# Performance work log

Hardware: AMD Instinct MI355X
Metric: run time of the kernel (lower is better)

The kernel has to match this reference:

```python
import jax, jax.numpy as jnp
import numpy as np

N = 30000          # num nodes
E = 480000         # num edges (before self-loops)
D_MODEL = 128
HEADS = 8
HEAD_DIM = D_MODEL // HEADS  # 16
LAYERS = 7
NUM_LABELS = 2
NEG_SLOPE = 0.2


def setup_inputs() -> dict:
    key = jax.random.key(0)
    ks = jax.random.split(key, 10)
    s = 0.05
    x = jax.random.normal(ks[0], (N, D_MODEL), dtype=jnp.float32)
    edge_index = jax.random.randint(ks[1], (2, E), 0, N, dtype=jnp.int64)
    Wl = jax.random.normal(ks[2], (LAYERS, D_MODEL, D_MODEL), dtype=jnp.float32) * s
    bl = jnp.zeros((LAYERS, D_MODEL), dtype=jnp.float32)
    Wr = jax.random.normal(ks[3], (LAYERS, D_MODEL, D_MODEL), dtype=jnp.float32) * s
    br = jnp.zeros((LAYERS, D_MODEL), dtype=jnp.float32)
    att = jax.random.normal(ks[4], (LAYERS, HEADS, HEAD_DIM), dtype=jnp.float32) * s
    bias = jnp.zeros((LAYERS, D_MODEL), dtype=jnp.float32)
    W_out = jax.random.normal(ks[5], (D_MODEL, 1), dtype=jnp.float32) * s
    b_out = jnp.zeros((1,), dtype=jnp.float32)
    return {"x": x, "edge_index": edge_index, "Wl": Wl, "bl": bl,
            "Wr": Wr, "br": br, "att": att, "bias": bias,
            "W_out": W_out, "b_out": b_out}


def _gatv2_layer(x, Wl, bl, Wr, br, att, bias, src, dst):
    # x: [N, d]; src/dst: [E'] (with self-loops). GATv2 (dropout off / eval).
    xl = (x @ Wl + bl).reshape(N, HEADS, HEAD_DIM)  # source transform
    xr = (x @ Wr + br).reshape(N, HEADS, HEAD_DIM)  # target transform
    m = xl[src] + xr[dst]                           # [E', H, D]
    e = jnp.einsum('ehd,hd->eh', jax.nn.leaky_relu(m, NEG_SLOPE), att)  # [E', H]
    # segment softmax over destination nodes (self-loops => no empty segments)
    emax = jax.ops.segment_max(e, dst, num_segments=N)  # [N, H]
    ee = jnp.exp(e - emax[dst])
    denom = jax.ops.segment_sum(ee, dst, num_segments=N)  # [N, H]
    alpha = ee / (denom[dst] + 1e-16)                      # [E', H]
    out = jax.ops.segment_sum(alpha[:, :, None] * xl[src], dst, num_segments=N)
    return out.reshape(N, D_MODEL) + bias


def reference(x, edge_index, Wl, bl, Wr, br, att, bias, W_out, b_out):
    loops = jnp.arange(N, dtype=edge_index.dtype)
    src = jnp.concatenate([edge_index[0], loops])  # add_self_loops=True (PyG default)
    dst = jnp.concatenate([edge_index[1], loops])
    for i in range(LAYERS):
        x = _gatv2_layer(x, Wl[i], bl[i], Wr[i], br[i], att[i], bias[i], src, dst)
    y = x @ W_out + b_out            # [N, 1]
    return y[:NUM_LABELS, 0].reshape(1, -1)  # [1, num_labels]
```

## Files before the change

### kernel.cpp

```cpp
#include <hip/hip_runtime.h>
#include <hip/hip_fp16.h>

#define NN 30000
#define ER 480000
#define ET 510000
#define D 128
#define NH 8
#define HD 16
#define NL 7
#define SLOPE 0.2f
#define NB_SCAN 118

typedef unsigned int uint32;
typedef unsigned short ushort;
typedef __attribute__((ext_vector_type(8))) short short8;
typedef __attribute__((ext_vector_type(4))) float f32x4;

__device__ inline ushort f2bf(float f) {
    uint32 u = __float_as_uint(f);
    return (ushort)((u + 0x7fffu + ((u >> 16) & 1u)) >> 16);
}
__device__ inline float bf2f(ushort h) {
    return __uint_as_float(((uint32)h) << 16);
}


__global__ void k_zero(int* __restrict__ p, int n) {
    int i = blockIdx.x * 256 + threadIdx.x;
    if (i < n) p[i] = 0;
}

__global__ void k_hist(const int* __restrict__ ei, int* __restrict__ counts) {
    int i = blockIdx.x * 256 + threadIdx.x;
    if (i >= ET) return;
    int dst = (i < ER) ? ei[ER + i] : (i - ER);
    atomicAdd(&counts[dst], 1);
}

__global__ __launch_bounds__(256) void k_scan1(const int* __restrict__ counts,
                                               int* __restrict__ offsets,
                                               int* __restrict__ partials) {
    int t = threadIdx.x;
    int i = blockIdx.x * 256 + t;
    int v = (i < NN) ? counts[i] : 0;
    int lane = t & 63;
    int incl = v;
#pragma unroll
    for (int d = 1; d < 64; d <<= 1) {
        int u = __shfl_up(incl, d);
        if (lane >= d) incl += u;
    }
    __shared__ int ws[4];
    if (lane == 63) ws[t >> 6] = incl;
    __syncthreads();
    int wid = t >> 6;
    int base = 0;
    if (wid > 0) base += ws[0];
    if (wid > 1) base += ws[1];
    if (wid > 2) base += ws[2];
    if (i < NN) offsets[i] = base + incl - v;
    if (t == 255) partials[blockIdx.x] = base + incl;
}

__global__ __launch_bounds__(128) void k_scan2(int* __restrict__ partials,
                                               int* __restrict__ offsets) {
    int t = threadIdx.x;
    int v = (t < NB_SCAN) ? partials[t] : 0;
    int lane = t & 63;
    int incl = v;
#pragma unroll
    for (int d = 1; d < 64; d <<= 1) {
        int u = __shfl_up(incl, d);
        if (lane >= d) incl += u;
    }
    __shared__ int w0;
    if (t == 63) w0 = incl;
    __syncthreads();
    int base = (t >= 64) ? w0 : 0;
    if (t < NB_SCAN) partials[t] = base + incl - v;
    if (t == 127) offsets[NN] = base + incl;
}

__global__ void k_scan3(const int* __restrict__ partials, int* __restrict__ offsets,
                        int* __restrict__ cursor) {
    int i = blockIdx.x * 256 + threadIdx.x;
    if (i < NN) {
        int o = offsets[i] + partials[blockIdx.x];
        offsets[i] = o;
        cursor[i] = o;
    }
}

__global__ void k_scatter(const int* __restrict__ ei, int* __restrict__ cursor,
                          int* __restrict__ srcs) {
    int i = blockIdx.x * 256 + threadIdx.x;
    if (i >= ET) return;
    int src, dst;
    if (i < ER) { src = ei[i]; dst = ei[ER + i]; }
    else        { src = i - ER; dst = src; }
    int pos = atomicAdd(&cursor[dst], 1);
    srcs[pos] = src;
}


__global__ __launch_bounds__(256) void k_wprep(const float* __restrict__ Wl,
                                               const float* __restrict__ Wr,
                                               ushort* __restrict__ Wth,
                                               ushort* __restrict__ Wtl) {
    int bx = blockIdx.x;
    int layer = bx >> 3;
    int n0 = (bx & 7) * 32;
    const float* WL = Wl + (size_t)layer * D * D;
    const float* WR = Wr + (size_t)layer * D * D;
    ushort* th = Wth + (size_t)layer * 256 * 128;
    ushort* tl = Wtl + (size_t)layer * 256 * 128;
    for (int idx = threadIdx.x; idx < 32 * 128; idx += 256) {
        int n = n0 + (idx >> 7);
        int k = idx & 127;
        float w = (n < 128) ? WL[k * 128 + n] : WR[k * 128 + (n - 128)];
        ushort h = f2bf(w);
        ushort e = f2bf(w - bf2f(h));
        th[n * 128 + k] = h;
        tl[n * 128 + k] = e;
    }
}


__global__ void k_xsplit(const float* __restrict__ x,
                         ushort* __restrict__ xh, ushort* __restrict__ xe) {
    int i = (blockIdx.x * 256 + threadIdx.x) * 4;
    if (i >= NN * D) return;
    float4 f = *reinterpret_cast<const float4*>(x + i);
    ushort4 h, e;
    h.x = f2bf(f.x); e.x = f2bf(f.x - bf2f(h.x));
    h.y = f2bf(f.y); e.y = f2bf(f.y - bf2f(h.y));
    h.z = f2bf(f.z); e.z = f2bf(f.z - bf2f(h.z));
    h.w = f2bf(f.w); e.w = f2bf(f.w - bf2f(h.w));
    *reinterpret_cast<ushort4*>(xh + i) = h;
    *reinterpret_cast<ushort4*>(xe + i) = e;
}


__global__ __launch_bounds__(256) void k_mm(const ushort* __restrict__ Xh,
                                            const ushort* __restrict__ Xe,
                                            const ushort* __restrict__ Wth,
                                            const ushort* __restrict__ Wtl,
                                            const float* __restrict__ bl,
                                            const float* __restrict__ br,
                                            ushort* __restrict__ xlh,
                                            float* __restrict__ xr) {
    __shared__ ushort Wh[64][136];
    __shared__ ushort We[64][136];
    const int row0 = blockIdx.x * 64;
    const int tid = threadIdx.x;
    const int wv = tid >> 6;
    const int l  = tid & 63;
    const int lr = l & 15;
    const int kg = (l >> 4) * 8;

    short8 Ah[4], Ae[4];
    {
        int row = row0 + wv * 16 + lr; if (row >= NN) row = NN - 1;
        const ushort* xh = Xh + (size_t)row * D;
        const ushort* xe = Xe + (size_t)row * D;
#pragma unroll
        for (int kc = 0; kc < 4; ++kc) {
            Ah[kc] = *reinterpret_cast<const short8*>(xh + kc * 32 + kg);
            Ae[kc] = *reinterpret_cast<const short8*>(xe + kc * 32 + kg);
        }
    }
    const int rbase = row0 + wv * 16 + (l >> 4) * 4;
    const int nn = tid >> 2;
    const int ch = tid & 3;

#pragma unroll
    for (int nq = 0; nq < 4; ++nq) {
        __syncthreads();
        {
            const ushort* wh = Wth + (size_t)(nq * 64 + nn) * 128;
            const ushort* wl = Wtl + (size_t)(nq * 64 + nn) * 128;
#pragma unroll
            for (int pass = 0; pass < 4; ++pass) {
                int ko = (ch * 4 + pass) * 8;
                *reinterpret_cast<uint4*>(&Wh[nn][ko]) = *reinterpret_cast<const uint4*>(wh + ko);
                *reinterpret_cast<uint4*>(&We[nn][ko]) = *reinterpret_cast<const uint4*>(wl + ko);
            }
        }
        __syncthreads();
        f32x4 acc[4] = {};
#pragma unroll
        for (int kc = 0; kc < 4; ++kc) {
#pragma unroll
            for (int nc = 0; nc < 4; ++nc) {
                short8 Bh = *reinterpret_cast<const short8*>(&Wh[nc * 16 + lr][kc * 32 + kg]);
                short8 Be = *reinterpret_cast<const short8*>(&We[nc * 16 + lr][kc * 32 + kg]);
                acc[nc] = __builtin_amdgcn_mfma_f32_16x16x32_bf16(Ah[kc], Bh, acc[nc], 0, 0, 0);
                acc[nc] = __builtin_amdgcn_mfma_f32_16x16x32_bf16(Ah[kc], Be, acc[nc], 0, 0, 0);
                acc[nc] = __builtin_amdgcn_mfma_f32_16x16x32_bf16(Ae[kc], Bh, acc[nc], 0, 0, 0);
            }
        }
#pragma unroll
        for (int nc = 0; nc < 4; ++nc) {
            int g = nq * 64 + nc * 16 + lr;
            if (g < 128) {
                float bb = bl[g];
#pragma unroll
                for (int j = 0; j < 4; ++j) {
                    int row = rbase + j;
                    if (row < NN)
                        xlh[(size_t)row * D + g] = __half_as_ushort(__float2half_rn(acc[nc][j] + bb));
                }
            } else {
                float bb = br[g - 128];
#pragma unroll
                for (int j = 0; j < 4; ++j) {
                    int row = rbase + j;
                    if (row < NN)
                        xr[(size_t)row * D + (g - 128)] = acc[nc][j] + bb;
                }
            }
        }
    }
}


#define FUSED_UPD(vv, sS, aS0, aS1)                                             \
    {                                                                           \
        float2 vf = __half22float2(*reinterpret_cast<const __half2*>(&(vv)));   \
        float v0 = vf.x, v1 = vf.y;                                             \
        float t0 = v0 + r0;                                                     \
        float t1 = v1 + r1;                                                     \
        float e = (fmaxf(t0, 0.f) + SLOPE * fminf(t0, 0.f)) * a0               \
                + (fmaxf(t1, 0.f) + SLOPE * fminf(t1, 0.f)) * a1;              \
        e += __shfl_xor(e, 1);                                                  \
        e += __shfl_xor(e, 2);                                                  \
        e += __shfl_xor(e, 4);                                                  \
        float p = __expf(e);                                                    \
        sS += p;                                                                \
        aS0 = fmaf(p, v0, aS0);                                                 \
        aS1 = fmaf(p, v1, aS1);                                                 \
    }

__global__ __launch_bounds__(256) void k_fused(const int* __restrict__ offsets,
                                               const int* __restrict__ srcs,
                                               const uint32* __restrict__ xlh,
                                               const float* __restrict__ xr,
                                               const float* __restrict__ att,
                                               const float* __restrict__ bias,
                                               uint32* __restrict__ outH,
                                               uint32* __restrict__ outE) {
    const int lane = threadIdx.x & 63;
    const int n = blockIdx.x * 4 + (threadIdx.x >> 6);
    const int off = offsets[n];
    const int deg = offsets[n + 1] - off;

    float2 rr = *reinterpret_cast<const float2*>(&xr[(size_t)n * D + 2 * lane]);
    const float r0 = rr.x, r1 = rr.y;
    float2 aa = *reinterpret_cast<const float2*>(&att[2 * lane]);
    const float a0 = aa.x, a1 = aa.y;

    float sA = 0.f, accA0 = 0.f, accA1 = 0.f;
    float sB = 0.f, accB0 = 0.f, accB1 = 0.f;

    int i = 0;
    int peel = (4 - (off & 3)) & 3;
    if (peel > deg) peel = deg;
    for (; i < peel; ++i) {
        uint32 vv = xlh[(size_t)srcs[off + i] * 64 + lane];
        FUSED_UPD(vv, sA, accA0, accA1);
    }
    for (; i + 8 <= deg; i += 8) {
        int4 sq0 = *reinterpret_cast<const int4*>(&srcs[off + i]);
        int4 sq1 = *reinterpret_cast<const int4*>(&srcs[off + i + 4]);
        int sa[8] = {sq0.x, sq0.y, sq0.z, sq0.w, sq1.x, sq1.y, sq1.z, sq1.w};
        uint32 vv[8];
#pragma unroll
        for (int j = 0; j < 8; ++j) vv[j] = xlh[(size_t)sa[j] * 64 + lane];
        FUSED_UPD(vv[0], sA, accA0, accA1);
        FUSED_UPD(vv[1], sB, accB0, accB1);
        FUSED_UPD(vv[2], sA, accA0, accA1);
        FUSED_UPD(vv[3], sB, accB0, accB1);
        FUSED_UPD(vv[4], sA, accA0, accA1);
        FUSED_UPD(vv[5], sB, accB0, accB1);
        FUSED_UPD(vv[6], sA, accA0, accA1);
        FUSED_UPD(vv[7], sB, accB0, accB1);
    }
    for (; i + 4 <= deg; i += 4) {
        int4 sq = *reinterpret_cast<const int4*>(&srcs[off + i]);
        int sa[4] = {sq.x, sq.y, sq.z, sq.w};
        uint32 vv[4];
#pragma unroll
        for (int j = 0; j < 4; ++j) vv[j] = xlh[(size_t)sa[j] * 64 + lane];
        FUSED_UPD(vv[0], sA, accA0, accA1);
        FUSED_UPD(vv[1], sB, accB0, accB1);
        FUSED_UPD(vv[2], sA, accA0, accA1);
        FUSED_UPD(vv[3], sB, accB0, accB1);
    }
    for (; i < deg; ++i) {
        uint32 vv = xlh[(size_t)srcs[off + i] * 64 + lane];
        FUSED_UPD(vv, sA, accA0, accA1);
    }

    float s = sA + sB;
    float inv = 1.f / (s + 1e-16f);
    float2 bb = *reinterpret_cast<const float2*>(&bias[2 * lane]);
    float o0 = (accA0 + accB0) * inv + bb.x;
    float o1 = (accA1 + accB1) * inv + bb.y;
    ushort h0 = f2bf(o0), h1 = f2bf(o1);
    ushort e0 = f2bf(o0 - bf2f(h0)), e1 = f2bf(o1 - bf2f(h1));
    outH[(size_t)n * 64 + lane] = (uint32)h0 | ((uint32)h1 << 16);
    outE[(size_t)n * 64 + lane] = (uint32)e0 | ((uint32)e1 << 16);
}


__global__ void k_out(const ushort* __restrict__ xh, const ushort* __restrict__ xe,
                      const float* __restrict__ Wout, const float* __restrict__ bout,
                      float* __restrict__ y) {
    int lane = threadIdx.x;
#pragma unroll
    for (int i = 0; i < 2; ++i) {
        float x0 = bf2f(xh[i * D + lane]) + bf2f(xe[i * D + lane]);
        float x1 = bf2f(xh[i * D + 64 + lane]) + bf2f(xe[i * D + 64 + lane]);
        float v = x0 * Wout[lane] + x1 * Wout[64 + lane];
        v += __shfl_xor(v, 1); v += __shfl_xor(v, 2); v += __shfl_xor(v, 4);
        v += __shfl_xor(v, 8); v += __shfl_xor(v, 16); v += __shfl_xor(v, 32);
        if (lane == 0) y[i] = v + bout[0];
    }
}


extern "C" void kernel_launch(void* const* d_in, const int* in_sizes, int n_in,
                              void* d_out, int out_size, void* d_ws, size_t ws_size,
                              hipStream_t stream) {
    const float* x_in = (const float*)d_in[0];
    const int*   ei   = (const int*)d_in[1];
    const float* Wl   = (const float*)d_in[2];
    const float* bl   = (const float*)d_in[3];
    const float* Wr   = (const float*)d_in[4];
    const float* br   = (const float*)d_in[5];
    const float* att  = (const float*)d_in[6];
    const float* bias = (const float*)d_in[7];
    const float* Wout = (const float*)d_in[8];
    const float* bout = (const float*)d_in[9];
    float* y = (float*)d_out;

    char* ws = (char*)d_ws;
    size_t o = 0;
    auto alloc = [&](size_t bytes) -> void* {
        void* p = ws + o;
        o = (o + bytes + 255) & ~(size_t)255;
        return p;
    };
    ushort* XhA = (ushort*)alloc((size_t)NN * D * 2);
    ushort* XeA = (ushort*)alloc((size_t)NN * D * 2);
    ushort* XhB = (ushort*)alloc((size_t)NN * D * 2);
    ushort* XeB = (ushort*)alloc((size_t)NN * D * 2);
    ushort* xlh = (ushort*)alloc((size_t)NN * D * 2);
    float*  xr  = (float*)alloc((size_t)NN * D * 4);
    ushort* Wth = (ushort*)alloc((size_t)NL * 256 * 128 * 2);
    ushort* Wtl = (ushort*)alloc((size_t)NL * 256 * 128 * 2);
    int* counts   = (int*)alloc((size_t)NN * 4);
    int* offsets  = (int*)alloc(((size_t)NN + 1) * 4);
    int* cursor   = (int*)alloc((size_t)NN * 4);
    int* srcs     = (int*)alloc((size_t)ET * 4);
    int* partials = (int*)alloc(256 * 4);
    (void)ws_size; (void)in_sizes; (void)n_in; (void)out_size;

    k_zero<<<NB_SCAN, 256, 0, stream>>>(counts, NN);
    k_hist<<<(ET + 255) / 256, 256, 0, stream>>>(ei, counts);
    k_scan1<<<NB_SCAN, 256, 0, stream>>>(counts, offsets, partials);
    k_scan2<<<1, 128, 0, stream>>>(partials, offsets);
    k_scan3<<<NB_SCAN, 256, 0, stream>>>(partials, offsets, cursor);
    k_scatter<<<(ET + 255) / 256, 256, 0, stream>>>(ei, cursor, srcs);
    k_wprep<<<NL * 8, 256, 0, stream>>>(Wl, Wr, Wth, Wtl);
    k_xsplit<<<NN * D / 1024, 256, 0, stream>>>(x_in, XhA, XeA);

    const int mgrid = (NN + 63) / 64;
    for (int i = 0; i < NL; ++i) {
        const ushort* inH = (i & 1) ? XhB : XhA;
        const ushort* inE = (i & 1) ? XeB : XeA;
        ushort* oH = (i & 1) ? XhA : XhB;
        ushort* oE = (i & 1) ? XeA : XeB;
        k_mm<<<mgrid, 256, 0, stream>>>(inH, inE,
                                        Wth + (size_t)i * 256 * 128,
                                        Wtl + (size_t)i * 256 * 128,
                                        bl + i * D, br + i * D, xlh, xr);
        k_fused<<<NN / 4, 256, 0, stream>>>(offsets, srcs, (const uint32*)xlh, xr,
                                            att + i * NH * HD, bias + i * D,
                                            (uint32*)oH, (uint32*)oE);
    }
    k_out<<<1, 64, 0, stream>>>(XhB, XeB, Wout, bout, y);
}
```

Measured before the change: 446.6 us.

## Split GEMM output quarters across blocks and compute attention scores in packed fp16

The projection GEMM now launches a 2D grid, so each block loads one 64-column weight quarter once and computes a single output tile instead of looping over four quarters with syncs. The target transform xr is stored as fp16 instead of fp32, which halves its write and read traffic. The fused attention kernel computes the add, leaky-relu and attention dot product with packed half2 math and fdot2. This cuts ALU work in the edge loop at the cost of fp16 rounding in the scores, and the 2D grid re-reads the X tile from memory four times.

Result: faster. 427.4 us (-4.3%).

```diff
diff --git a/kernel.cpp b/kernel.cpp
--- a/kernel.cpp
+++ b/kernel.cpp
@@ -15,6 +15,13 @@
 typedef unsigned short ushort;
 typedef __attribute__((ext_vector_type(8))) short short8;
 typedef __attribute__((ext_vector_type(4))) float f32x4;
+typedef _Float16 h2_t __attribute__((ext_vector_type(2)));
+
+#if defined(__has_builtin)
+#if __has_builtin(__builtin_amdgcn_fdot2)
+#define HAS_FDOT2 1
+#endif
+#endif
 
 __device__ inline ushort f2bf(float f) {
     uint32 u = __float_as_uint(f);
@@ -22,6 +29,21 @@
 }
 __device__ inline float bf2f(ushort h) {
     return __uint_as_float(((uint32)h) << 16);
+}
+
+__device__ inline __half2 hmax2p(__half2 a, __half2 b) {
+    h2_t x = *reinterpret_cast<h2_t*>(&a), y = *reinterpret_cast<h2_t*>(&b);
+    h2_t r;
+    r[0] = x[0] > y[0] ? x[0] : y[0];
+    r[1] = x[1] > y[1] ? x[1] : y[1];
+    return *reinterpret_cast<__half2*>(&r);
+}
+__device__ inline __half2 hmin2p(__half2 a, __half2 b) {
+    h2_t x = *reinterpret_cast<h2_t*>(&a), y = *reinterpret_cast<h2_t*>(&b);
+    h2_t r;
+    r[0] = x[0] < y[0] ? x[0] : y[0];
+    r[1] = x[1] < y[1] ? x[1] : y[1];
+    return *reinterpret_cast<__half2*>(&r);
 }
 
 
@@ -148,16 +170,29 @@
                                             const float* __restrict__ bl,
                                             const float* __restrict__ br,
                                             ushort* __restrict__ xlh,
-                                            float* __restrict__ xr) {
+                                            ushort* __restrict__ xrh) {
     __shared__ ushort Wh[64][136];
     __shared__ ushort We[64][136];
     const int row0 = blockIdx.x * 64;
+    const int nq = blockIdx.y;
     const int tid = threadIdx.x;
     const int wv = tid >> 6;
     const int l  = tid & 63;
     const int lr = l & 15;
     const int kg = (l >> 4) * 8;
 
+    {
+        int nn = tid >> 2;
+        int ch = tid & 3;
+        const ushort* wh = Wth + (size_t)(nq * 64 + nn) * 128;
+        const ushort* wl = Wtl + (size_t)(nq * 64 + nn) * 128;
+#pragma unroll
+        for (int pass = 0; pass < 4; ++pass) {
+            int ko = (ch * 4 + pass) * 8;
+            *reinterpret_cast<uint4*>(&Wh[nn][ko]) = *reinterpret_cast<const uint4*>(wh + ko);
+            *reinterpret_cast<uint4*>(&We[nn][ko]) = *reinterpret_cast<const uint4*>(wl + ko);
+        }
+    }
     short8 Ah[4], Ae[4];
     {
         int row = row0 + wv * 16 + lr; if (row >= NN) row = NN - 1;
@@ -169,82 +204,68 @@
             Ae[kc] = *reinterpret_cast<const short8*>(xe + kc * 32 + kg);
         }
     }
+    __syncthreads();
+
+    f32x4 acc[4] = {};
+#pragma unroll
+    for (int kc = 0; kc < 4; ++kc) {
+#pragma unroll
+        for (int nc = 0; nc < 4; ++nc) {
+            short8 Bh = *reinterpret_cast<const short8*>(&Wh[nc * 16 + lr][kc * 32 + kg]);
+            short8 Be = *reinterpret_cast<const short8*>(&We[nc * 16 + lr][kc * 32 + kg]);
+            acc[nc] = __builtin_amdgcn_mfma_f32_16x16x32_bf16(Ah[kc], Bh, acc[nc], 0, 0, 0);
+            acc[nc] = __builtin_amdgcn_mfma_f32_16x16x32_bf16(Ah[kc], Be, acc[nc], 0, 0, 0);
+            acc[nc] = __builtin_amdgcn_mfma_f32_16x16x32_bf16(Ae[kc], Bh, acc[nc], 0, 0, 0);
+        }
+    }
     const int rbase = row0 + wv * 16 + (l >> 4) * 4;
-    const int nn = tid >> 2;
-    const int ch = tid & 3;
-
-#pragma unroll
-    for (int nq = 0; nq < 4; ++nq) {
-        __syncthreads();
-        {
-            const ushort* wh = Wth + (size_t)(nq * 64 + nn) * 128;
-            const ushort* wl = Wtl + (size_t)(nq * 64 + nn) * 128;
-#pragma unroll
-            for (int pass = 0; pass < 4; ++pass) {
-                int ko = (ch * 4 + pass) * 8;
-                *reinterpret_cast<uint4*>(&Wh[nn][ko]) = *reinterpret_cast<const uint4*>(wh + ko);
-                *reinterpret_cast<uint4*>(&We[nn][ko]) = *reinterpret_cast<const uint4*>(wl + ko);
-            }
+#pragma unroll
+    for (int nc = 0; nc < 4; ++nc) {
+        int g = nq * 64 + nc * 16 + lr;
+        float bb = (g < 128) ? bl[g] : br[g - 128];
+        ushort* dst = (g < 128) ? (xlh + g) : (xrh + (g - 128));
+#pragma unroll
+        for (int j = 0; j < 4; ++j) {
+            int row = rbase + j;
+            if (row < NN)
+                dst[(size_t)row * D] = __half_as_ushort(__float2half_rn(acc[nc][j] + bb));
         }
-        __syncthreads();
-        f32x4 acc[4] = {};
-#pragma unroll
-        for (int kc = 0; kc < 4; ++kc) {
-#pragma unroll
-            for (int nc = 0; nc < 4; ++nc) {
-                short8 Bh = *reinterpret_cast<const short8*>(&Wh[nc * 16 + lr][kc * 32 + kg]);
-                short8 Be = *reinterpret_cast<const short8*>(&We[nc * 16 + lr][kc * 32 + kg]);
-                acc[nc] = __builtin_amdgcn_mfma_f32_16x16x32_bf16(Ah[kc], Bh, acc[nc], 0, 0, 0);
-                acc[nc] = __builtin_amdgcn_mfma_f32_16x16x32_bf16(Ah[kc], Be, acc[nc], 0, 0, 0);
-                acc[nc] = __builtin_amdgcn_mfma_f32_16x16x32_bf16(Ae[kc], Bh, acc[nc], 0, 0, 0);
-            }
-        }
-#pragma unroll
-        for (int nc = 0; nc < 4; ++nc) {
-            int g = nq * 64 + nc * 16 + lr;
-            if (g < 128) {
-                float bb = bl[g];
-#pragma unroll
-                for (int j = 0; j < 4; ++j) {
-                    int row = rbase + j;
-                    if (row < NN)
-                        xlh[(size_t)row * D + g] = __half_as_ushort(__float2half_rn(acc[nc][j] + bb));
-                }
-            } else {
-                float bb = br[g - 128];
-#pragma unroll
-                for (int j = 0; j < 4; ++j) {
-                    int row = rbase + j;
-                    if (row < NN)
-                        xr[(size_t)row * D + (g - 128)] = acc[nc][j] + bb;
-                }
-            }
-        }
-    }
-}
-
+    }
+}
+
+
+__device__ inline float score_dot(__half2 lr2, __half2 a2) {
+#ifdef HAS_FDOT2
+    h2_t x = *reinterpret_cast<h2_t*>(&lr2);
+    h2_t a = *reinterpret_cast<h2_t*>(&a2);
+    return __builtin_amdgcn_fdot2(x, a, 0.0f, false);
+#else
+    float2 lf = __half22float2(lr2);
+    float2 af = __half22float2(a2);
+    return fmaf(lf.x, af.x, lf.y * af.y);
+#endif
+}
 
 #define FUSED_UPD(vv, sS, aS0, aS1)                                             \
     {                                                                           \
-        float2 vf = __half22float2(*reinterpret_cast<const __half2*>(&(vv)));   \
-        float v0 = vf.x, v1 = vf.y;                                             \
-        float t0 = v0 + r0;                                                     \
-        float t1 = v1 + r1;                                                     \
-        float e = (fmaxf(t0, 0.f) + SLOPE * fminf(t0, 0.f)) * a0               \
-                + (fmaxf(t1, 0.f) + SLOPE * fminf(t1, 0.f)) * a1;              \
+        __half2 vh = *reinterpret_cast<const __half2*>(&(vv));                  \
+        __half2 th = __hadd2(vh, rh);                                           \
+        __half2 lr2 = __hfma2(hmin2p(th, zero2), slope2, hmax2p(th, zero2));    \
+        float e = score_dot(lr2, ah2);                                          \
         e += __shfl_xor(e, 1);                                                  \
         e += __shfl_xor(e, 2);                                                  \
         e += __shfl_xor(e, 4);                                                  \
         float p = __expf(e);                                                    \
+        float2 vf = __half22float2(vh);                                         \
         sS += p;                                                                \
-        aS0 = fmaf(p, v0, aS0);                                                 \
-        aS1 = fmaf(p, v1, aS1);                                                 \
+        aS0 = fmaf(p, vf.x, aS0);                                               \
+        aS1 = fmaf(p, vf.y, aS1);                                               \
     }
 
 __global__ __launch_bounds__(256) void k_fused(const int* __restrict__ offsets,
                                                const int* __restrict__ srcs,
                                                const uint32* __restrict__ xlh,
-                                               const float* __restrict__ xr,
+                                               const uint32* __restrict__ xrh,
                                                const float* __restrict__ att,
                                                const float* __restrict__ bias,
                                                uint32* __restrict__ outH,
@@ -254,10 +275,12 @@
     const int off = offsets[n];
     const int deg = offsets[n + 1] - off;
 
-    float2 rr = *reinterpret_cast<const float2*>(&xr[(size_t)n * D + 2 * lane]);
-    const float r0 = rr.x, r1 = rr.y;
+    uint32 ru = xrh[(size_t)n * 64 + lane];
+    const __half2 rh = *reinterpret_cast<const __half2*>(&ru);
     float2 aa = *reinterpret_cast<const float2*>(&att[2 * lane]);
-    const float a0 = aa.x, a1 = aa.y;
+    const __half2 ah2 = __floats2half2_rn(aa.x, aa.y);
+    const __half2 zero2 = __float2half2_rn(0.f);
+    const __half2 slope2 = __float2half2_rn(SLOPE);
 
     float sA = 0.f, accA0 = 0.f, accA1 = 0.f;
     float sB = 0.f, accB0 = 0.f, accB1 = 0.f;
@@ -356,7 +379,7 @@
     ushort* XhB = (ushort*)alloc((size_t)NN * D * 2);
     ushort* XeB = (ushort*)alloc((size_t)NN * D * 2);
     ushort* xlh = (ushort*)alloc((size_t)NN * D * 2);
-    float*  xr  = (float*)alloc((size_t)NN * D * 4);
+    ushort* xrh = (ushort*)alloc((size_t)NN * D * 2);
     ushort* Wth = (ushort*)alloc((size_t)NL * 256 * 128 * 2);
     ushort* Wtl = (ushort*)alloc((size_t)NL * 256 * 128 * 2);
     int* counts   = (int*)alloc((size_t)NN * 4);
@@ -381,11 +404,12 @@
         const ushort* inE = (i & 1) ? XeB : XeA;
         ushort* oH = (i & 1) ? XhA : XhB;
         ushort* oE = (i & 1) ? XeA : XeB;
-        k_mm<<<mgrid, 256, 0, stream>>>(inH, inE,
-                                        Wth + (size_t)i * 256 * 128,
-                                        Wtl + (size_t)i * 256 * 128,
-                                        bl + i * D, br + i * D, xlh, xr);
-        k_fused<<<NN / 4, 256, 0, stream>>>(offsets, srcs, (const uint32*)xlh, xr,
+        k_mm<<<dim3(mgrid, 4), 256, 0, stream>>>(inH, inE,
+                                                 Wth + (size_t)i * 256 * 128,
+                                                 Wtl + (size_t)i * 256 * 128,
+                                                 bl + i * D, br + i * D, xlh, xrh);
+        k_fused<<<NN / 4, 256, 0, stream>>>(offsets, srcs, (const uint32*)xlh,
+                                            (const uint32*)xrh,
                                             att + i * NH * HD, bias + i * D,
                                             (uint32*)oH, (uint32*)oE);
     }
```
